# Kernel tuning notes

Hardware: AMD Instinct MI355X
Metric: run time of the kernel (lower is better)

The kernel has to match this reference:

```python
import jax, jax.numpy as jnp
import numpy as np

N_NODES = 50000
N_EDGES = 1600000
SLOPE = 0.01  # LeakyReLU default negative slope


def _leaky(x):
    return jnp.where(x >= 0, x, SLOPE * x)


def _gcn(x, W, b, row, col, num_nodes):
    """PyG GCNConv: x' = D^{-1/2}(A+I)D^{-1/2} X W + b (self-loops already in row/col)."""
    x = x @ W  # [N, 64]
    deg = jax.ops.segment_sum(jnp.ones_like(row, dtype=x.dtype), col, num_segments=num_nodes)
    dinv = jnp.where(deg > 0, jax.lax.rsqrt(deg), 0.0)
    norm = dinv[row] * dinv[col]  # [E+N]
    msg = x[row] * norm[:, None]  # gather + scale, [E+N, 64]
    out = jax.ops.segment_sum(msg, col, num_segments=num_nodes)
    return out + b


def setup_inputs() -> dict:
    key = jax.random.key(0)
    ks = jax.random.split(key, 24)
    d = {}
    d["screen"] = jax.random.normal(ks[0], (N_NODES, 768), jnp.float32)
    d["des"] = jax.random.normal(ks[1], (N_NODES, 768), jnp.float32)
    d["tweet"] = jax.random.normal(ks[2], (N_NODES, 768), jnp.float32)
    d["profile"] = jax.random.normal(ks[3], (N_NODES, 5), jnp.float32)
    d["personal"] = jax.random.normal(ks[4], (N_NODES, 7), jnp.float32)
    d["edge"] = jax.random.randint(ks[5], (2, N_EDGES), 0, N_NODES, dtype=jnp.int32)

    def lin(k, fan_in, fan_out):
        s = 1.0 / np.sqrt(fan_in)
        k1, k2 = jax.random.split(k)
        W = jax.random.uniform(k1, (fan_in, fan_out), jnp.float32, -s, s)
        b = jax.random.uniform(k2, (fan_out,), jnp.float32, -s, s)
        return W, b

    d["W_screen"], d["b_screen"] = lin(ks[6], 768, 16)
    d["W_des"], d["b_des"] = lin(ks[7], 768, 16)
    d["W_tweet"], d["b_tweet"] = lin(ks[8], 768, 16)
    d["W_pro"], d["b_pro"] = lin(ks[9], 5, 8)
    d["W_per"], d["b_per"] = lin(ks[10], 7, 8)
    d["W_lin"], d["b_lin"] = lin(ks[11], 64, 64)
    d["W_g1"], d["b_g1"] = lin(ks[12], 64, 64)
    d["W_g2"], d["b_g2"] = lin(ks[13], 64, 64)
    d["W_g3"], d["b_g3"] = lin(ks[14], 64, 64)
    d["W_o1"], d["b_o1"] = lin(ks[15], 64, 64)
    d["W_o2"], d["b_o2"] = lin(ks[16], 64, 2)
    return d


def reference(screen, des, tweet, profile, personal, edge,
              W_screen, b_screen, W_des, b_des, W_tweet, b_tweet,
              W_pro, b_pro, W_per, b_per, W_lin, b_lin,
              W_g1, b_g1, W_g2, b_g2, W_g3, b_g3,
              W_o1, b_o1, W_o2, b_o2):
    n = screen.shape[0]
    # dropout layers act as identity in eval mode
    s = _leaky(screen @ W_screen + b_screen)
    de = _leaky(des @ W_des + b_des)
    t = _leaky(tweet @ W_tweet + b_tweet)
    p = _leaky(profile @ W_pro + b_pro)
    pe = _leaky(personal @ W_per + b_per)
    x1 = jnp.concatenate((s, de, t, p, pe), axis=1)  # [N, 64]
    x = _leaky(x1 @ W_lin + b_lin)
    # add self-loops once (shared by all three GCN layers)
    loops = jnp.arange(n, dtype=edge.dtype)
    row = jnp.concatenate([edge[0], loops])
    col = jnp.concatenate([edge[1], loops])
    x = _gcn(x, W_g1, b_g1, row, col, n) + x1
    x = _gcn(x, W_g2, b_g2, row, col, n) + x1
    x = _gcn(x, W_g3, b_g3, row, col, n) + x1
    x = _leaky(x @ W_o1 + b_o1)
    return jax.nn.sigmoid(x @ W_o2 + b_o2)
```

## Files before the change

### kernel.cpp

```cpp
#include <hip/hip_runtime.h>

__device__ __forceinline__ float leaky(float v) { return v >= 0.f ? v : 0.01f * v; }

__device__ __forceinline__ void fma4(float4& a, float s, const float4& w) {
    a.x = fmaf(s, w.x, a.x); a.y = fmaf(s, w.y, a.y);
    a.z = fmaf(s, w.z, a.z); a.w = fmaf(s, w.w, a.w);
}

__device__ __forceinline__ unsigned short f2bf(float x) {
    unsigned b = __float_as_uint(x);
    return (unsigned short)((b + 0x7FFFu + ((b >> 16) & 1u)) >> 16);
}
__device__ __forceinline__ float bf2f(unsigned short u) {
    return __uint_as_float(((unsigned)u) << 16);
}

typedef __attribute__((ext_vector_type(8))) short short8v;
typedef __attribute__((ext_vector_type(4))) float float4v;

__global__ __launch_bounds__(256) void k_scan_part(const int* __restrict__ deg,
                                                   int* __restrict__ part,
                                                   int* __restrict__ bsum, int N) {
    __shared__ int tmp[256];
    int tid = threadIdx.x;
    int i = blockIdx.x * 256 + tid;
    int v = (i < N) ? deg[i] : 0;
    tmp[tid] = v;
    __syncthreads();
    for (int ofs = 1; ofs < 256; ofs <<= 1) {
        int t = (tid >= ofs) ? tmp[tid - ofs] : 0;
        __syncthreads();
        tmp[tid] += t;
        __syncthreads();
    }
    int incl = tmp[tid];
    if (i < N) part[i] = incl - v;
    if (tid == 255) bsum[blockIdx.x] = incl;
}

__global__ __launch_bounds__(256) void k_scan_sums(const int* __restrict__ bsum,
                                                   int* __restrict__ boff, int NB,
                                                   int* __restrict__ offs_last) {
    __shared__ int tmp[256];
    int tid = threadIdx.x;
    int v = (tid < NB) ? bsum[tid] : 0;
    tmp[tid] = v;
    __syncthreads();
    for (int ofs = 1; ofs < 256; ofs <<= 1) {
        int t = (tid >= ofs) ? tmp[tid - ofs] : 0;
        __syncthreads();
        tmp[tid] += t;
        __syncthreads();
    }
    int incl = tmp[tid];
    if (tid < NB) boff[tid] = incl - v;
    if (tid == 255) offs_last[0] = incl;
}

__global__ __launch_bounds__(256) void k_scan_final(const int* __restrict__ part,
                                                    const int* __restrict__ boff,
                                                    const int* __restrict__ deg,
                                                    int* __restrict__ offs,
                                                    int* __restrict__ pos,
                                                    float* __restrict__ dinv, int N) {
    int i = blockIdx.x * 256 + threadIdx.x;
    if (i < N) {
        int o = part[i] + boff[blockIdx.x];
        offs[i] = o;
        pos[i] = o;
        dinv[i] = rsqrtf((float)(deg[i] + 1));
    }
}

__global__ __launch_bounds__(512) void k_featB(
    const float* __restrict__ s, const float* __restrict__ d, const float* __restrict__ t,
    const float* __restrict__ Ws, const float* __restrict__ bs2,
    const float* __restrict__ Wd, const float* __restrict__ bd2,
    const float* __restrict__ Wt, const float* __restrict__ bt2,
    const float* __restrict__ prof, const float* __restrict__ pers,
    const float* __restrict__ Wp, const float* __restrict__ bp,
    const float* __restrict__ Wpe, const float* __restrict__ bpe,
    const int* __restrict__ colv, int* __restrict__ deg, int E,
    float* __restrict__ x1g, int N, int NG, int NSM) {
    __shared__ short8v wfv[3072];

    const int bid = blockIdx.x;
    const int tid = threadIdx.x;

    if (bid >= 3 * NG + NSM) {
        int e = (bid - 3 * NG - NSM) * 512 + tid;
        if (e < E) atomicAdd(&deg[colv[e]], 1);
        return;
    }

    if (bid >= 3 * NG) {
        int n = (bid - 3 * NG) * 512 + tid;
        if (n >= N) return;
        float pv[5], pe[7];
#pragma unroll
        for (int i = 0; i < 5; ++i) pv[i] = prof[(size_t)n * 5 + i];
#pragma unroll
        for (int i = 0; i < 7; ++i) pe[i] = pers[(size_t)n * 7 + i];
        float o[16];
#pragma unroll
        for (int j = 0; j < 8; ++j) {
            float a = bp[j];
#pragma unroll
            for (int i = 0; i < 5; ++i) a = fmaf(pv[i], Wp[i * 8 + j], a);
            o[j] = leaky(a);
            float a2 = bpe[j];
#pragma unroll
            for (int i = 0; i < 7; ++i) a2 = fmaf(pe[i], Wpe[i * 8 + j], a2);
            o[8 + j] = leaky(a2);
        }
#pragma unroll
        for (int v = 0; v < 4; ++v)
            *reinterpret_cast<float4*>(x1g + (size_t)n * 64 + 48 + v * 4) =
                make_float4(o[v * 4], o[v * 4 + 1], o[v * 4 + 2], o[v * 4 + 3]);
        return;
    }

    const int f = bid / NG;
    const int grp = bid - f * NG;
    const float* __restrict__ X = (f == 0) ? s : ((f == 1) ? d : t);
    const float* __restrict__ W = (f == 0) ? Ws : ((f == 1) ? Wd : Wt);
    const float* __restrict__ B = (f == 0) ? bs2 : ((f == 1) ? bd2 : bt2);
    const int n0 = grp * 128;
    const int lane = tid & 63;
    const int wid = tid >> 6;

    short* wfs = (short*)wfv;
#pragma unroll
    for (int v = 0; v < 6; ++v) {
        int idx4 = tid + v * 512;
        float4 w4 = *reinterpret_cast<const float4*>(W + (size_t)idx4 * 4);
        int k = idx4 >> 2;
        int j0 = (idx4 & 3) * 4;
        int c = k >> 5, g = (k >> 3) & 3, i = k & 7;
        float wq[4] = {w4.x, w4.y, w4.z, w4.w};
#pragma unroll
        for (int q = 0; q < 4; ++q) {
            int sl = (c * 64 + g * 16 + j0 + q) * 8 + i;
            unsigned short h = f2bf(wq[q]);
            wfs[sl] = (short)h;
            wfs[12288 + sl] = (short)f2bf(wq[q] - bf2f(h));
        }
    }
    __syncthreads();

    const int nb = n0 + wid * 16;
    int mrow = nb + (lane & 15); if (mrow >= N) mrow = N - 1;
    const float* base = X + (size_t)mrow * 768 + ((lane >> 4) << 3);

    float4 pa[4], pb[4];
#pragma unroll
    for (int u = 0; u < 4; ++u) {
        pa[u] = *reinterpret_cast<const float4*>(base + u * 32);
        pb[u] = *reinterpret_cast<const float4*>(base + u * 32 + 4);
    }
    float4v acc = {0.f, 0.f, 0.f, 0.f};

#pragma unroll
    for (int c = 0; c < 24; ++c) {
        const int u = c & 3;
        float xs[8] = {pa[u].x, pa[u].y, pa[u].z, pa[u].w,
                       pb[u].x, pb[u].y, pb[u].z, pb[u].w};
        if (c + 4 < 24) {
            pa[u] = *reinterpret_cast<const float4*>(base + (c + 4) * 32);
            pb[u] = *reinterpret_cast<const float4*>(base + (c + 4) * 32 + 4);
        }
        short8v xh, xl;
#pragma unroll
        for (int i = 0; i < 8; ++i) {
            unsigned short h = f2bf(xs[i]);
            xh[i] = (short)h;
            xl[i] = (short)f2bf(xs[i] - bf2f(h));
        }
        short8v wh = wfv[c * 64 + lane];
        short8v wl = wfv[1536 + c * 64 + lane];
        acc = __builtin_amdgcn_mfma_f32_16x16x32_bf16(xh, wh, acc, 0, 0, 0);
        acc = __builtin_amdgcn_mfma_f32_16x16x32_bf16(xl, wh, acc, 0, 0, 0);
        acc = __builtin_amdgcn_mfma_f32_16x16x32_bf16(xh, wl, acc, 0, 0, 0);
    }

    int j = lane & 15;
    float bb = B[j];
#pragma unroll
    for (int r = 0; r < 4; ++r) {
        int n = nb + ((lane >> 4) << 2) + r;
        if (n < N) x1g[(size_t)n * 64 + f * 16 + j] = leaky(acc[r] + bb);
    }
}

__global__ __launch_bounds__(256) void k_lin1(const float* __restrict__ x1,
                                              const float* __restrict__ Wl,
                                              const float* __restrict__ bl,
                                              const float* __restrict__ Wg1,
                                              const float* __restrict__ dinvv,
                                              const int* __restrict__ rowv,
                                              const int* __restrict__ colv,
                                              int* __restrict__ pos,
                                              int* __restrict__ csr, int E,
                                              unsigned short* __restrict__ z,
                                              int N, int NGB) {
    __shared__ float4 xt4[1024];
    __shared__ float4 wt4[1024];
    const int tid = threadIdx.x;
    const int bid = blockIdx.x;

    if (bid >= NGB) {
        int e = (bid - NGB) * 256 + tid;
        if (e < E) {
            int p = atomicAdd(&pos[colv[e]], 1);
            csr[p] = rowv[e];
        }
        return;
    }

    const int n0 = bid * 64;
    const int nq = tid & 15;
    const int jq = tid >> 4;

#pragma unroll
    for (int v = 0; v < 4; ++v) {
        int L = v * 256 + tid;
        int n = L >> 4, c4 = L & 15;
        int nn = n0 + n; if (nn >= N) nn = N - 1;
        xt4[n * 16 + (c4 ^ (n & 15))] = *reinterpret_cast<const float4*>(x1 + (size_t)nn * 64 + c4 * 4);
        wt4[L] = *reinterpret_cast<const float4*>(Wl + (size_t)L * 4);
    }
    __syncthreads();

    float4 acc[4];
#pragma unroll
    for (int g = 0; g < 4; ++g) acc[g] = make_float4(0.f, 0.f, 0.f, 0.f);
    for (int k = 0; k < 64; k += 4) {
        float4 w0 = wt4[(k + 0) * 16 + jq];
        float4 w1 = wt4[(k + 1) * 16 + jq];
        float4 w2 = wt4[(k + 2) * 16 + jq];
        float4 w3 = wt4[(k + 3) * 16 + jq];
        int k4 = k >> 2;
#pragma unroll
        for (int g = 0; g < 4; ++g) {
            int n = nq + (g << 4);
            float4 xv = xt4[n * 16 + (k4 ^ (n & 15))];
            fma4(acc[g], xv.x, w0);
            fma4(acc[g], xv.y, w1);
            fma4(acc[g], xv.z, w2);
            fma4(acc[g], xv.w, w3);
        }
    }
    float4 bb = *reinterpret_cast<const float4*>(bl + jq * 4);
    __syncthreads();

#pragma unroll
    for (int g = 0; g < 4; ++g) {
        int n = nq + (g << 4);
        float4 h;
        h.x = leaky(acc[g].x + bb.x);
        h.y = leaky(acc[g].y + bb.y);
        h.z = leaky(acc[g].z + bb.z);
        h.w = leaky(acc[g].w + bb.w);
        xt4[n * 16 + (jq ^ (n & 15))] = h;
    }
#pragma unroll
    for (int v = 0; v < 4; ++v) {
        int L = v * 256 + tid;
        wt4[L] = *reinterpret_cast<const float4*>(Wg1 + (size_t)L * 4);
    }
    __syncthreads();

#pragma unroll
    for (int g = 0; g < 4; ++g) acc[g] = make_float4(0.f, 0.f, 0.f, 0.f);
    for (int k = 0; k < 64; k += 4) {
        float4 w0 = wt4[(k + 0) * 16 + jq];
        float4 w1 = wt4[(k + 1) * 16 + jq];
        float4 w2 = wt4[(k + 2) * 16 + jq];
        float4 w3 = wt4[(k + 3) * 16 + jq];
        int k4 = k >> 2;
#pragma unroll
        for (int g = 0; g < 4; ++g) {
            int n = nq + (g << 4);
            float4 xv = xt4[n * 16 + (k4 ^ (n & 15))];
            fma4(acc[g], xv.x, w0);
            fma4(acc[g], xv.y, w1);
            fma4(acc[g], xv.z, w2);
            fma4(acc[g], xv.w, w3);
        }
    }
#pragma unroll
    for (int g = 0; g < 4; ++g) {
        int n = nq + (g << 4);
        if (n0 + n >= N) continue;
        float dv = dinvv[n0 + n];
        ushort4 o;
        o.x = f2bf(acc[g].x * dv); o.y = f2bf(acc[g].y * dv);
        o.z = f2bf(acc[g].z * dv); o.w = f2bf(acc[g].w * dv);
        *reinterpret_cast<ushort4*>(z + (size_t)(n0 + n) * 64 + jq * 4) = o;
    }
}

__global__ __launch_bounds__(256, 4) void k_mm64(const float* __restrict__ xin,
                                                 const float* __restrict__ W,
                                                 const float* __restrict__ dinvv,
                                                 unsigned short* __restrict__ z, int N) {
    __shared__ float4 xt4[1024];
    __shared__ float4 wt4[1024];
    const int tid = threadIdx.x;
    const int n0 = blockIdx.x * 64;
#pragma unroll
    for (int v = 0; v < 4; ++v) {
        int L = v * 256 + tid;
        int n = L >> 4, c4 = L & 15;
        int nn = n0 + n; if (nn >= N) nn = N - 1;
        xt4[n * 16 + (c4 ^ (n & 15))] = *reinterpret_cast<const float4*>(xin + (size_t)nn * 64 + c4 * 4);
        wt4[L] = *reinterpret_cast<const float4*>(W + (size_t)L * 4);
    }
    __syncthreads();
    const int nq = tid & 15;
    const int jq = tid >> 4;
    float4 acc[4];
#pragma unroll
    for (int g = 0; g < 4; ++g) acc[g] = make_float4(0.f, 0.f, 0.f, 0.f);
    for (int k = 0; k < 64; k += 4) {
        float4 w0 = wt4[(k + 0) * 16 + jq];
        float4 w1 = wt4[(k + 1) * 16 + jq];
        float4 w2 = wt4[(k + 2) * 16 + jq];
        float4 w3 = wt4[(k + 3) * 16 + jq];
        int k4 = k >> 2;
#pragma unroll
        for (int g = 0; g < 4; ++g) {
            int n = nq + (g << 4);
            float4 xv = xt4[n * 16 + (k4 ^ (n & 15))];
            fma4(acc[g], xv.x, w0);
            fma4(acc[g], xv.y, w1);
            fma4(acc[g], xv.z, w2);
            fma4(acc[g], xv.w, w3);
        }
    }
#pragma unroll
    for (int g = 0; g < 4; ++g) {
        int n = nq + (g << 4);
        if (n0 + n >= N) continue;
        float dv = dinvv[n0 + n];
        ushort4 o;
        o.x = f2bf(acc[g].x * dv); o.y = f2bf(acc[g].y * dv);
        o.z = f2bf(acc[g].z * dv); o.w = f2bf(acc[g].w * dv);
        *reinterpret_cast<ushort4*>(z + (size_t)(n0 + n) * 64 + jq * 4) = o;
    }
}

__global__ __launch_bounds__(256) void k_agg(const unsigned short* __restrict__ z,
                                             const int* __restrict__ offs,
                                             const int* __restrict__ csr,
                                             const float* __restrict__ dinv,
                                             const float* __restrict__ bias,
                                             const float* __restrict__ x1,
                                             float* __restrict__ xout, int N) {
    int lane = threadIdx.x & 63;
    int c = blockIdx.x * 4 + (threadIdx.x >> 6);
    if (c >= N) return;
    int s = __builtin_amdgcn_readfirstlane(offs[c]);
    int e = __builtin_amdgcn_readfirstlane(offs[c + 1]);
    const int half = lane >> 5;
    const int d = lane & 31;
    const unsigned* __restrict__ zr = (const unsigned*)z;

    float ax = 0.f, ay = 0.f;
    if (half == 0) {
        unsigned sv = zr[(size_t)c * 32 + d];
        ax = bf2f((unsigned short)(sv & 0xffffu));
        ay = bf2f((unsigned short)(sv >> 16));
    }
    float ux[8] = {0, 0, 0, 0, 0, 0, 0, 0};
    float uy[8] = {0, 0, 0, 0, 0, 0, 0, 0};
    int j = s;
    for (; j + 16 <= e; j += 16) {
#pragma unroll
        for (int u = 0; u < 8; ++u) {
            int r0 = csr[j + 2 * u];
            int r1 = csr[j + 2 * u + 1];
            int r = half ? r1 : r0;
            unsigned v = zr[(size_t)r * 32 + d];
            ux[u] += bf2f((unsigned short)(v & 0xffffu));
            uy[u] += bf2f((unsigned short)(v >> 16));
        }
    }
    for (; j + 2 <= e; j += 2) {
        int r0 = csr[j];
        int r1 = csr[j + 1];
        int r = half ? r1 : r0;
        unsigned v = zr[(size_t)r * 32 + d];
        ax += bf2f((unsigned short)(v & 0xffffu));
        ay += bf2f((unsigned short)(v >> 16));
    }
    if (j < e && half == 0) {
        int r = csr[j];
        unsigned v = zr[(size_t)r * 32 + d];
        ax += bf2f((unsigned short)(v & 0xffffu));
        ay += bf2f((unsigned short)(v >> 16));
    }
    float tx = ax + ((ux[0] + ux[1]) + (ux[2] + ux[3])) + ((ux[4] + ux[5]) + (ux[6] + ux[7]));
    float ty = ay + ((uy[0] + uy[1]) + (uy[2] + uy[3])) + ((uy[4] + uy[5]) + (uy[6] + uy[7]));
    tx += __shfl_xor(tx, 32);
    ty += __shfl_xor(ty, 32);
    if (half == 0) {
        float dv = dinv[c];
        float2 bb = reinterpret_cast<const float2*>(bias)[d];
        float2 xx = *reinterpret_cast<const float2*>(x1 + (size_t)c * 64 + 2 * d);
        float2 o;
        o.x = dv * tx + bb.x + xx.x;
        o.y = dv * ty + bb.y + xx.y;
        *reinterpret_cast<float2*>(xout + (size_t)c * 64 + 2 * d) = o;
    }
}

__global__ __launch_bounds__(256) void k_head(const float* __restrict__ xin,
                                              const float* __restrict__ Wo1,
                                              const float* __restrict__ bo1,
                                              const float* __restrict__ Wo2,
                                              const float* __restrict__ bo2,
                                              float* __restrict__ out, int N) {
    __shared__ float xsg[64][65];
    __shared__ float wg[64][65];
    __shared__ float hs[64][65];
    __shared__ float wo2[128];
    const int tid = threadIdx.x;
    const int n0 = blockIdx.x * 64;
#pragma unroll
    for (int v = 0; v < 4; ++v) {
        int idx = tid + v * 256;
        int n = idx >> 4;
        int jj = (idx & 15) << 2;
        float4 xv = make_float4(0.f, 0.f, 0.f, 0.f);
        if (n0 + n < N) xv = *reinterpret_cast<const float4*>(xin + (size_t)(n0 + n) * 64 + jj);
        xsg[n][jj] = xv.x; xsg[n][jj + 1] = xv.y; xsg[n][jj + 2] = xv.z; xsg[n][jj + 3] = xv.w;
        float4 w = *reinterpret_cast<const float4*>(Wo1 + (size_t)n * 64 + jj);
        wg[n][jj] = w.x; wg[n][jj + 1] = w.y; wg[n][jj + 2] = w.z; wg[n][jj + 3] = w.w;
    }
    if (tid < 128) wo2[tid] = Wo2[tid];
    __syncthreads();
    int j = tid & 63;
    int g = tid >> 6;
    float bj = bo1[j];
    for (int i = 0; i < 16; ++i) {
        int n = g * 16 + i;
        float a = bj;
#pragma unroll
        for (int k = 0; k < 64; ++k) a += xsg[n][k] * wg[k][j];
        hs[n][j] = leaky(a);
    }
    __syncthreads();
    if (tid < 128) {
        int n = tid >> 1;
        int j2 = tid & 1;
        float a = bo2[j2];
#pragma unroll
        for (int k = 0; k < 64; ++k) a += hs[n][k] * wo2[k * 2 + j2];
        if (n0 + n < N) out[(size_t)(n0 + n) * 2 + j2] = 1.f / (1.f + expf(-a));
    }
}

extern "C" void kernel_launch(void* const* d_in, const int* in_sizes, int n_in,
                              void* d_out, int out_size, void* d_ws, size_t ws_size,
                              hipStream_t stream) {
    const float* screen   = (const float*)d_in[0];
    const float* des      = (const float*)d_in[1];
    const float* tweet    = (const float*)d_in[2];
    const float* profile  = (const float*)d_in[3];
    const float* personal = (const float*)d_in[4];
    const int*   edge     = (const int*)d_in[5];
    const float* Ws  = (const float*)d_in[6],  *bs  = (const float*)d_in[7];
    const float* Wd  = (const float*)d_in[8],  *bd  = (const float*)d_in[9];
    const float* Wt  = (const float*)d_in[10], *bt  = (const float*)d_in[11];
    const float* Wp  = (const float*)d_in[12], *bp  = (const float*)d_in[13];
    const float* Wpe = (const float*)d_in[14], *bpe = (const float*)d_in[15];
    const float* Wl  = (const float*)d_in[16], *bl  = (const float*)d_in[17];
    const float* Wg1 = (const float*)d_in[18], *bg1 = (const float*)d_in[19];
    const float* Wg2 = (const float*)d_in[20], *bg2 = (const float*)d_in[21];
    const float* Wg3 = (const float*)d_in[22], *bg3 = (const float*)d_in[23];
    const float* Wo1 = (const float*)d_in[24], *bo1 = (const float*)d_in[25];
    const float* Wo2 = (const float*)d_in[26], *bo2 = (const float*)d_in[27];

    const int N = in_sizes[0] / 768;
    const int E = in_sizes[5] / 2;
    const int* row = edge;
    const int* col = edge + E;

    size_t off = 0;
    auto alloc = [&](size_t bytes) -> void* {
        void* p = (char*)d_ws + off;
        off += (bytes + 255) & ~(size_t)255;
        return p;
    };
    const size_t NF = (size_t)N * 64;
    float* x1   = (float*)alloc(NF * 4);
    float* xa   = (float*)alloc(NF * 4);
    float* xb   = (float*)alloc(NF * 4);
    unsigned short* z = (unsigned short*)alloc(NF * 2);
    float* dinv = (float*)alloc((size_t)N * 4);
    int* deg  = (int*)alloc((size_t)N * 4);
    int* part = (int*)alloc((size_t)N * 4);
    int* offs = (int*)alloc((size_t)(N + 1) * 4);
    int* pos  = (int*)alloc((size_t)N * 4);
    int* csr  = (int*)alloc((size_t)E * 4);
    const int NB = (N + 255) / 256;
    int* bsum = (int*)alloc((size_t)NB * 4);
    int* boff = (int*)alloc((size_t)NB * 4);
    (void)ws_size; (void)n_in; (void)out_size;

    hipMemsetAsync(deg, 0, (size_t)N * 4, stream);

    const int NG = (N + 127) / 128;
    const int NSM = (N + 511) / 512;
    const int NDEG = (E + 511) / 512;
    k_featB<<<NG * 3 + NSM + NDEG, 512, 0, stream>>>(screen, des, tweet,
                                                     Ws, bs, Wd, bd, Wt, bt,
                                                     profile, personal, Wp, bp, Wpe, bpe,
                                                     col, deg, E,
                                                     x1, N, NG, NSM);

    k_scan_part<<<NB, 256, 0, stream>>>(deg, part, bsum, N);
    k_scan_sums<<<1, 256, 0, stream>>>(bsum, boff, NB, offs + N);
    k_scan_final<<<NB, 256, 0, stream>>>(part, boff, deg, offs, pos, dinv, N);

    const int NGB = (N + 63) / 64;
    const int NFILL = (E + 255) / 256;
    const int NAB = (N + 3) / 4;
    k_lin1<<<NGB + NFILL, 256, 0, stream>>>(x1, Wl, bl, Wg1, dinv,
                                            row, col, pos, csr, E, z, N, NGB);
    k_agg<<<NAB, 256, 0, stream>>>(z, offs, csr, dinv, bg1, x1, xb, N);
    k_mm64<<<NGB, 256, 0, stream>>>(xb, Wg2, dinv, z, N);
    k_agg<<<NAB, 256, 0, stream>>>(z, offs, csr, dinv, bg2, x1, xa, N);
    k_mm64<<<NGB, 256, 0, stream>>>(xa, Wg3, dinv, z, N);
    k_agg<<<NAB, 256, 0, stream>>>(z, offs, csr, dinv, bg3, x1, xb, N);

    k_head<<<NGB, 256, 0, stream>>>(xb, Wo1, bo1, Wo2, bo2, (float*)d_out, N);
}
```

Before: 475.3 us.

## Fold edge degree and CSR-fill work into compute blocks; add sched barriers

```diff
diff --git a/kernel.cpp b/kernel.cpp
--- a/kernel.cpp
+++ b/kernel.cpp
@@ -87,10 +87,13 @@
     const int bid = blockIdx.x;
     const int tid = threadIdx.x;
 
-    if (bid >= 3 * NG + NSM) {
-        int e = (bid - 3 * NG - NSM) * 512 + tid;
-        if (e < E) atomicAdd(&deg[colv[e]], 1);
-        return;
+    {
+        const int NW = 3 * NG + NSM;
+        int eper = (E + NW - 1) / NW;
+        int ebase = bid * eper;
+        int eend = ebase + eper; if (eend > E) eend = E;
+        for (int e = ebase + tid; e < eend; e += 512)
+            atomicAdd(&deg[colv[e]], 1);
     }
 
     if (bid >= 3 * NG) {
@@ -158,6 +161,7 @@
         pa[u] = *reinterpret_cast<const float4*>(base + u * 32);
         pb[u] = *reinterpret_cast<const float4*>(base + u * 32 + 4);
     }
+    __builtin_amdgcn_sched_barrier(0);
     float4v acc = {0.f, 0.f, 0.f, 0.f};
 
 #pragma unroll
@@ -181,6 +185,7 @@
         acc = __builtin_amdgcn_mfma_f32_16x16x32_bf16(xh, wh, acc, 0, 0, 0);
         acc = __builtin_amdgcn_mfma_f32_16x16x32_bf16(xl, wh, acc, 0, 0, 0);
         acc = __builtin_amdgcn_mfma_f32_16x16x32_bf16(xh, wl, acc, 0, 0, 0);
+        __builtin_amdgcn_sched_barrier(0);
     }
 
     int j = lane & 15;
@@ -208,13 +213,24 @@
     const int tid = threadIdx.x;
     const int bid = blockIdx.x;
 
-    if (bid >= NGB) {
-        int e = (bid - NGB) * 256 + tid;
-        if (e < E) {
-            int p = atomicAdd(&pos[colv[e]], 1);
-            csr[p] = rowv[e];
-        }
-        return;
+    {
+        int eper = (E + NGB - 1) / NGB;
+        int ebase = bid * eper;
+        int eend = ebase + eper; if (eend > E) eend = E;
+        int cols[8], rows[8];
+#pragma unroll
+        for (int r = 0; r < 8; ++r) {
+            int e = ebase + tid + r * 256;
+            cols[r] = (e < eend) ? colv[e] : -1;
+            rows[r] = (e < eend) ? rowv[e] : 0;
+        }
+        int ps[8];
+#pragma unroll
+        for (int r = 0; r < 8; ++r)
+            if (cols[r] >= 0) ps[r] = atomicAdd(&pos[cols[r]], 1);
+#pragma unroll
+        for (int r = 0; r < 8; ++r)
+            if (cols[r] >= 0) csr[ps[r]] = rows[r];
     }
 
     const int n0 = bid * 64;
@@ -513,22 +529,20 @@
 
     const int NG = (N + 127) / 128;
     const int NSM = (N + 511) / 512;
-    const int NDEG = (E + 511) / 512;
-    k_featB<<<NG * 3 + NSM + NDEG, 512, 0, stream>>>(screen, des, tweet,
-                                                     Ws, bs, Wd, bd, Wt, bt,
-                                                     profile, personal, Wp, bp, Wpe, bpe,
-                                                     col, deg, E,
-                                                     x1, N, NG, NSM);
+    k_featB<<<NG * 3 + NSM, 512, 0, stream>>>(screen, des, tweet,
+                                              Ws, bs, Wd, bd, Wt, bt,
+                                              profile, personal, Wp, bp, Wpe, bpe,
+                                              col, deg, E,
+                                              x1, N, NG, NSM);
 
     k_scan_part<<<NB, 256, 0, stream>>>(deg, part, bsum, N);
     k_scan_sums<<<1, 256, 0, stream>>>(bsum, boff, NB, offs + N);
     k_scan_final<<<NB, 256, 0, stream>>>(part, boff, deg, offs, pos, dinv, N);
 
     const int NGB = (N + 63) / 64;
-    const int NFILL = (E + 255) / 256;
     const int NAB = (N + 3) / 4;
-    k_lin1<<<NGB + NFILL, 256, 0, stream>>>(x1, Wl, bl, Wg1, dinv,
-                                            row, col, pos, csr, E, z, N, NGB);
+    k_lin1<<<NGB, 256, 0, stream>>>(x1, Wl, bl, Wg1, dinv,
+                                    row, col, pos, csr, E, z, N, NGB);
     k_agg<<<NAB, 256, 0, stream>>>(z, offs, csr, dinv, bg1, x1, xb, N);
     k_mm64<<<NGB, 256, 0, stream>>>(xb, Wg2, dinv, z, N);
     k_agg<<<NAB, 256, 0, stream>>>(z, offs, csr, dinv, bg2, x1, xa, N);
```

Measured after the change: 467.5 us. No clear change (-1.6%).
